# Optimization experiments

Hardware: AMD Instinct MI355X
Metric: run time of the kernel (lower is better)

The kernel has to match this reference:

```python
import jax, jax.numpy as jnp
import numpy as np

ALPHA = 0.2  # LeakyReLU negative slope
B, N, F_IN, F_OUT = 8, 2048, 256, 64


def setup_inputs() -> dict:
    key = jax.random.key(0)
    k1, k2, k3, k4 = jax.random.split(key, 4)
    x = jax.random.normal(k1, (B, N, F_IN), dtype=jnp.float32)
    adj = jax.random.randint(k2, (B, N, N), 0, 2, dtype=jnp.int32)
    # xavier_uniform with gain=1.414
    gain = 1.414
    lim_W = gain * np.sqrt(6.0 / (F_IN + F_OUT))
    W = jax.random.uniform(k3, (F_IN, F_OUT), dtype=jnp.float32, minval=-lim_W, maxval=lim_W)
    lim_a = gain * np.sqrt(6.0 / (2 * F_OUT + 1))
    a = jax.random.uniform(k4, (2 * F_OUT, 1), dtype=jnp.float32, minval=-lim_a, maxval=lim_a)
    return {"x": x, "adj": adj, "W": W, "a": a}


def reference(x, adj, W, a):
    h = jnp.einsum('bni,io->bno', x, W)  # [B, N, F_OUT]
    f_out = W.shape[1]
    # additive score a^T [h_i ; h_j] = (h_i . a_left) + (h_j . a_right)
    a_left = a[:f_out, 0]   # [F_OUT]
    a_right = a[f_out:, 0]  # [F_OUT]
    e_l = h @ a_left   # [B, N]
    e_r = h @ a_right  # [B, N]
    e = e_l[:, :, None] + e_r[:, None, :]          # [B, N, N]
    e = jnp.where(e > 0, e, ALPHA * e)             # LeakyReLU
    e = jnp.where(adj > 0, e, jnp.float32(-9e15))  # adjacency mask
    attention = jax.nn.softmax(e, axis=2)          # [B, N, N]
    h_prime = jnp.einsum('bnm,bmo->bno', attention, h)  # [B, N, F_OUT]
    return jax.nn.elu(h_prime)
```

## Files before the change

kernel.cpp:

```cpp
#include <hip/hip_runtime.h>
#include <math.h>

#define BATCH 8
#define NN 2048
#define FIN 256
#define FOUT 64
#define ALPHA 0.2f

typedef __attribute__((ext_vector_type(8))) short bf16x8;
typedef __attribute__((ext_vector_type(4))) float f32x4;

static __device__ __forceinline__ unsigned short f2bf(float f) {
  unsigned int u = __float_as_uint(f);
  u += 0x7fffu + ((u >> 16) & 1u);
  return (unsigned short)(u >> 16);
}
static __device__ __forceinline__ float bf2f(unsigned short h) {
  return __uint_as_float(((unsigned int)h) << 16);
}
static __device__ __forceinline__ void gload16(const void* g, void* l) {
  __builtin_amdgcn_global_load_lds(
      (const __attribute__((address_space(1))) unsigned int*)g,
      (__attribute__((address_space(3))) unsigned int*)l, 16, 0, 0);
}

__global__ __launch_bounds__(256) void k1_h(
    const float* __restrict__ x, const float* __restrict__ W,
    const float* __restrict__ a, float* __restrict__ el,
    float* __restrict__ er, unsigned char* __restrict__ hS) {
  __shared__ __align__(16) unsigned short lds[32768];
  const int t = threadIdx.x;
  const int wv = t >> 6;
  const int l = t & 63;
  const int l15 = l & 15;
  const int kg = l >> 4;

  {
    const float4* W4 = (const float4*)W;
    #pragma unroll
    for (int i = 0; i < 16; ++i) {
      int f = t + i * 256;
      float4 v = W4[f];
      int k = f >> 4;
      int ob = (f & 15) * 4;
      float vv[4] = {v.x, v.y, v.z, v.w};
      #pragma unroll
      for (int c = 0; c < 4; ++c) {
        int o = ob + c;
        unsigned short hi = f2bf(vv[c]);
        unsigned short lo = f2bf(vv[c] - bf2f(hi));
        int idx = o * 256 + (((k >> 3) ^ (o & 7)) * 8) + (k & 7);
        lds[idx] = hi;
        lds[16384 + idx] = lo;
      }
    }
  }
  __syncthreads();

  const int row = blockIdx.x * 64 + wv * 16 + l15;
  f32x4 acc[4] = {{0.f,0.f,0.f,0.f},{0.f,0.f,0.f,0.f},
                  {0.f,0.f,0.f,0.f},{0.f,0.f,0.f,0.f}};
  const float* xrow = x + (size_t)row * FIN;

  #pragma unroll
  for (int ks = 0; ks < 8; ++ks) {
    int k0 = ks * 32;
    float4 xa = *(const float4*)(xrow + k0 + kg * 8);
    float4 xb = *(const float4*)(xrow + k0 + kg * 8 + 4);
    float xv[8] = {xa.x, xa.y, xa.z, xa.w, xb.x, xb.y, xb.z, xb.w};
    bf16x8 ahi, alo;
    #pragma unroll
    for (int j = 0; j < 8; ++j) {
      unsigned short hi = f2bf(xv[j]);
      unsigned short lo = f2bf(xv[j] - bf2f(hi));
      ahi[j] = (short)hi;
      alo[j] = (short)lo;
    }
    int kgidx = ks * 4 + kg;
    #pragma unroll
    for (int ot = 0; ot < 4; ++ot) {
      int o = ot * 16 + l15;
      int base = o * 256 + ((kgidx ^ (o & 7)) * 8);
      bf16x8 bhi = *(const bf16x8*)&lds[base];
      bf16x8 blo = *(const bf16x8*)&lds[16384 + base];
      acc[ot] = __builtin_amdgcn_mfma_f32_16x16x32_bf16(ahi, bhi, acc[ot], 0, 0, 0);
      acc[ot] = __builtin_amdgcn_mfma_f32_16x16x32_bf16(ahi, blo, acc[ot], 0, 0, 0);
      acc[ot] = __builtin_amdgcn_mfma_f32_16x16x32_bf16(alo, bhi, acc[ot], 0, 0, 0);
    }
  }

  float aLv[4], aRv[4];
  #pragma unroll
  for (int ot = 0; ot < 4; ++ot) {
    aLv[ot] = a[ot * 16 + l15];
    aRv[ot] = a[64 + ot * 16 + l15];
  }
  #pragma unroll
  for (int jj = 0; jj < 4; ++jj) {
    float pl = 0.f, pr = 0.f;
    #pragma unroll
    for (int ot = 0; ot < 4; ++ot) {
      pl += acc[ot][jj] * aLv[ot];
      pr += acc[ot][jj] * aRv[ot];
    }
    #pragma unroll
    for (int s = 1; s < 16; s <<= 1) {
      pl += __shfl_xor(pl, s);
      pr += __shfl_xor(pr, s);
    }
    if (l15 == 0) {
      int grow = blockIdx.x * 64 + wv * 16 + kg * 4 + jj;
      el[grow] = pl;
      er[grow] = pr;
    }
  }

  __syncthreads();
  #pragma unroll
  for (int ot = 0; ot < 4; ++ot) {
    int o = ot * 16 + l15;
    int xorv = (o >> 1) & 3;
    #pragma unroll
    for (int jj = 0; jj < 4; ++jj) {
      int m_loc = wv * 16 + kg * 4 + jj;
      int ks2 = m_loc >> 5;
      int kg2 = (m_loc >> 3) & 3;
      int j = m_loc & 7;
      int kgp = kg2 ^ xorv;
      float v = acc[ot][jj];
      unsigned short hi = f2bf(v);
      unsigned short lo = f2bf(v - bf2f(hi));
      int base = ((ks2 * 2 + 0) * 64 + o) * 32 + kgp * 8 + j;
      lds[base] = hi;
      lds[base + 2048] = lo;
    }
  }
  __syncthreads();

  {
    const uint4* src = (const uint4*)(const void*)lds;
    uint4* dst = (uint4*)(hS + (size_t)blockIdx.x * 16384);
    #pragma unroll
    for (int i = 0; i < 4; ++i) dst[t + i * 256] = src[t + i * 256];
  }
}

__global__ __launch_bounds__(256, 2) void k2_attn(
    const int* __restrict__ adj, const unsigned char* __restrict__ hS,
    const float* __restrict__ el, const float* __restrict__ er,
    float* __restrict__ out) {
  __shared__ __align__(1024) unsigned char buf[2][2][16384];
  const int t = threadIdx.x;
  const int wv = t >> 6;
  const int l = t & 63;
  const int l15 = l & 15;
  const int kg = l >> 4;
  const int pair = wv >> 1;
  const int pw = wv & 1;

  int bid = blockIdx.x;
  int swz = (bid & 7) * 64 + (bid >> 3);
  int b = swz >> 6;
  int n0 = (swz & 63) * 32;
  const int nrow = n0 + pw * 16 + l15;

  const float eL = el[b * NN + nrow];
  const float* erp = er + b * NN + pair * 1024;
  const int* arow = adj + (size_t)b * NN * NN + (size_t)nrow * NN + pair * 1024;
  const unsigned char* hSb =
      hS + (size_t)b * 32 * 16384 + (size_t)pair * 16 * 16384;

  const int laneoff = l15 * 64 + ((kg ^ ((l >> 1) & 3)) * 16);

  f32x4 acc[4] = {{0.f,0.f,0.f,0.f},{0.f,0.f,0.f,0.f},
                  {0.f,0.f,0.f,0.f},{0.f,0.f,0.f,0.f}};
  float Sacc = 0.f;

  #pragma unroll
  for (int s = 0; s < 8; ++s) {
    int seg = pw * 8 + s;
    gload16(hSb + seg * 1024 + l * 16, &buf[pair][0][seg * 1024]);
  }
  int4 av[4];
  float4 ev[4];
  #pragma unroll
  for (int ksx = 0; ksx < 2; ++ksx) {
    av[ksx * 2 + 0] = *(const int4*)(arow + ksx * 32 + kg * 8);
    av[ksx * 2 + 1] = *(const int4*)(arow + ksx * 32 + kg * 8 + 4);
    ev[ksx * 2 + 0] = *(const float4*)(erp + ksx * 32 + kg * 8);
    ev[ksx * 2 + 1] = *(const float4*)(erp + ksx * 32 + kg * 8 + 4);
  }
  __syncthreads();

  for (int tc = 0; tc < 16; ++tc) {
    const unsigned char* cur = &buf[pair][tc & 1][0];
    int4 avn[4];
    float4 evn[4];
    if (tc < 15) {
      const unsigned char* src = hSb + (size_t)(tc + 1) * 16384;
      unsigned char* dstb = &buf[pair][(tc + 1) & 1][0];
      #pragma unroll
      for (int s = 0; s < 8; ++s) {
        int seg = pw * 8 + s;
        gload16(src + seg * 1024 + l * 16, dstb + seg * 1024);
      }
      int mb = (tc + 1) * 64;
      #pragma unroll
      for (int ksx = 0; ksx < 2; ++ksx) {
        avn[ksx * 2 + 0] = *(const int4*)(arow + mb + ksx * 32 + kg * 8);
        avn[ksx * 2 + 1] = *(const int4*)(arow + mb + ksx * 32 + kg * 8 + 4);
        evn[ksx * 2 + 0] = *(const float4*)(erp + mb + ksx * 32 + kg * 8);
        evn[ksx * 2 + 1] = *(const float4*)(erp + mb + ksx * 32 + kg * 8 + 4);
      }
    }

    #pragma unroll
    for (int ks = 0; ks < 2; ++ks) {
      int aarr[8] = {av[ks*2].x, av[ks*2].y, av[ks*2].z, av[ks*2].w,
                     av[ks*2+1].x, av[ks*2+1].y, av[ks*2+1].z, av[ks*2+1].w};
      float earr[8] = {ev[ks*2].x, ev[ks*2].y, ev[ks*2].z, ev[ks*2].w,
                       ev[ks*2+1].x, ev[ks*2+1].y, ev[ks*2+1].z, ev[ks*2+1].w};
      bf16x8 af;
      #pragma unroll
      for (int j = 0; j < 8; ++j) {
        float e = eL + earr[j];
        e = fmaxf(e, ALPHA * e);
        float w = (aarr[j] > 0) ? __expf(e) : 0.f;
        unsigned short hb = f2bf(w);
        af[j] = (short)hb;
        Sacc += bf2f(hb);
      }
      #pragma unroll
      for (int ot = 0; ot < 4; ++ot) {
        const unsigned char* p = cur + ks * 8192 + ot * 1024 + laneoff;
        bf16x8 bhi = *(const bf16x8*)p;
        bf16x8 blo = *(const bf16x8*)(p + 4096);
        acc[ot] = __builtin_amdgcn_mfma_f32_16x16x32_bf16(af, bhi, acc[ot], 0, 0, 0);
        acc[ot] = __builtin_amdgcn_mfma_f32_16x16x32_bf16(af, blo, acc[ot], 0, 0, 0);
      }
    }

    if (tc < 15) {
      #pragma unroll
      for (int i = 0; i < 4; ++i) { av[i] = avn[i]; ev[i] = evn[i]; }
    }
    __syncthreads();
  }

  float Sred = Sacc + __shfl_xor(Sacc, 16);
  Sred += __shfl_xor(Sred, 32);

  {
    unsigned char* cb = &buf[0][0][0];
    const int slot = pw * 64 + l;
    if (pair == 1) {
      float* dst = (float*)(cb + slot * 96);
      *(f32x4*)(dst + 0)  = acc[0];
      *(f32x4*)(dst + 4)  = acc[1];
      *(f32x4*)(dst + 8)  = acc[2];
      *(f32x4*)(dst + 12) = acc[3];
      dst[16] = Sred;
    }
    __syncthreads();
    if (pair == 1) return;
    const float* src = (const float*)(cb + slot * 96);
    #pragma unroll
    for (int ot = 0; ot < 4; ++ot) {
      f32x4 o4 = *(const f32x4*)(src + ot * 4);
      acc[ot] += o4;
    }
    Sred += src[16];
  }

  float Sj[4];
  #pragma unroll
  for (int jj = 0; jj < 4; ++jj) Sj[jj] = __shfl(Sred, kg * 4 + jj);
  #pragma unroll
  for (int ot = 0; ot < 4; ++ot) {
    #pragma unroll
    for (int jj = 0; jj < 4; ++jj) {
      float v = acc[ot][jj] / Sj[jj];
      float res = v > 0.f ? v : expm1f(v);
      out[((size_t)b * NN + n0 + pw * 16 + kg * 4 + jj) * FOUT + ot * 16 + l15] = res;
    }
  }
}

extern "C" void kernel_launch(void* const* d_in, const int* in_sizes, int n_in,
                              void* d_out, int out_size, void* d_ws, size_t ws_size,
                              hipStream_t stream) {
  const float* x   = (const float*)d_in[0];
  const int*   adj = (const int*)d_in[1];
  const float* W   = (const float*)d_in[2];
  const float* a   = (const float*)d_in[3];
  float* out = (float*)d_out;

  unsigned char* hS = (unsigned char*)d_ws;
  float* el = (float*)(hS + (size_t)BATCH * 32 * 16384);
  float* er = el + BATCH * NN;

  hipLaunchKernelGGL(k1_h, dim3(256), dim3(256), 0, stream, x, W, a, el, er, hS);
  hipLaunchKernelGGL(k2_attn, dim3(512), dim3(256), 0, stream, adj, hS, el, er, out);
}
```

Measured before the change: 52.57 us.

## Deepen adjacency/score register prefetch to two stages with manual vmcnt waits

```diff
diff --git a/kernel.cpp b/kernel.cpp
--- a/kernel.cpp
+++ b/kernel.cpp
@@ -176,50 +176,51 @@
                   {0.f,0.f,0.f,0.f},{0.f,0.f,0.f,0.f}};
   float Sacc = 0.f;
 
-  #pragma unroll
-  for (int s = 0; s < 8; ++s) {
-    int seg = pw * 8 + s;
-    gload16(hSb + seg * 1024 + l * 16, &buf[pair][0][seg * 1024]);
-  }
-  int4 av[4];
-  float4 ev[4];
-  #pragma unroll
-  for (int ksx = 0; ksx < 2; ++ksx) {
-    av[ksx * 2 + 0] = *(const int4*)(arow + ksx * 32 + kg * 8);
-    av[ksx * 2 + 1] = *(const int4*)(arow + ksx * 32 + kg * 8 + 4);
-    ev[ksx * 2 + 0] = *(const float4*)(erp + ksx * 32 + kg * 8);
-    ev[ksx * 2 + 1] = *(const float4*)(erp + ksx * 32 + kg * 8 + 4);
-  }
-  __syncthreads();
-
+  int4 av0[4], av1[4], av2[4];
+  float4 ev0[4], ev1[4], ev2[4];
+
+#define STAGE(tcc) {                                                       \
+    const unsigned char* src_ = hSb + (size_t)(tcc) * 16384;               \
+    unsigned char* dst_ = &buf[pair][(tcc) & 1][0];                        \
+    _Pragma("unroll")                                                      \
+    for (int s_ = 0; s_ < 8; ++s_) {                                       \
+      int seg_ = pw * 8 + s_;                                              \
+      gload16(src_ + seg_ * 1024 + l * 16, dst_ + seg_ * 1024);            \
+    } }
+
+#define LOADR(A, E, tcc) {                                                 \
+    int mb_ = (tcc) * 64;                                                  \
+    _Pragma("unroll")                                                      \
+    for (int kx_ = 0; kx_ < 2; ++kx_) {                                    \
+      A[kx_*2+0] = *(const int4*)(arow + mb_ + kx_*32 + kg*8);             \
+      A[kx_*2+1] = *(const int4*)(arow + mb_ + kx_*32 + kg*8 + 4);         \
+      E[kx_*2+0] = *(const float4*)(erp + mb_ + kx_*32 + kg*8);            \
+      E[kx_*2+1] = *(const float4*)(erp + mb_ + kx_*32 + kg*8 + 4);        \
+    } }
+
+  STAGE(0);
+  LOADR(av0, ev0, 0);
+  LOADR(av1, ev1, 1);
+  asm volatile("s_waitcnt vmcnt(0)" ::: "memory");
+  __builtin_amdgcn_s_barrier();
+
+  #pragma unroll
   for (int tc = 0; tc < 16; ++tc) {
+    if (tc < 15) STAGE(tc + 1);
+    if (tc < 14) LOADR(av2, ev2, tc + 2);
+
+    if (tc < 14)      { asm volatile("s_waitcnt vmcnt(16)" ::: "memory"); }
+    else if (tc < 15) { asm volatile("s_waitcnt vmcnt(8)"  ::: "memory"); }
+    else              { asm volatile("s_waitcnt vmcnt(0)"  ::: "memory"); }
+    __builtin_amdgcn_s_barrier();
+
     const unsigned char* cur = &buf[pair][tc & 1][0];
-    int4 avn[4];
-    float4 evn[4];
-    if (tc < 15) {
-      const unsigned char* src = hSb + (size_t)(tc + 1) * 16384;
-      unsigned char* dstb = &buf[pair][(tc + 1) & 1][0];
-      #pragma unroll
-      for (int s = 0; s < 8; ++s) {
-        int seg = pw * 8 + s;
-        gload16(src + seg * 1024 + l * 16, dstb + seg * 1024);
-      }
-      int mb = (tc + 1) * 64;
-      #pragma unroll
-      for (int ksx = 0; ksx < 2; ++ksx) {
-        avn[ksx * 2 + 0] = *(const int4*)(arow + mb + ksx * 32 + kg * 8);
-        avn[ksx * 2 + 1] = *(const int4*)(arow + mb + ksx * 32 + kg * 8 + 4);
-        evn[ksx * 2 + 0] = *(const float4*)(erp + mb + ksx * 32 + kg * 8);
-        evn[ksx * 2 + 1] = *(const float4*)(erp + mb + ksx * 32 + kg * 8 + 4);
-      }
-    }
-
     #pragma unroll
     for (int ks = 0; ks < 2; ++ks) {
-      int aarr[8] = {av[ks*2].x, av[ks*2].y, av[ks*2].z, av[ks*2].w,
-                     av[ks*2+1].x, av[ks*2+1].y, av[ks*2+1].z, av[ks*2+1].w};
-      float earr[8] = {ev[ks*2].x, ev[ks*2].y, ev[ks*2].z, ev[ks*2].w,
-                       ev[ks*2+1].x, ev[ks*2+1].y, ev[ks*2+1].z, ev[ks*2+1].w};
+      int aarr[8] = {av0[ks*2].x, av0[ks*2].y, av0[ks*2].z, av0[ks*2].w,
+                     av0[ks*2+1].x, av0[ks*2+1].y, av0[ks*2+1].z, av0[ks*2+1].w};
+      float earr[8] = {ev0[ks*2].x, ev0[ks*2].y, ev0[ks*2].z, ev0[ks*2].w,
+                       ev0[ks*2+1].x, ev0[ks*2+1].y, ev0[ks*2+1].z, ev0[ks*2+1].w};
       bf16x8 af;
       #pragma unroll
       for (int j = 0; j < 8; ++j) {
@@ -240,11 +241,14 @@
       }
     }
 
-    if (tc < 15) {
-      #pragma unroll
-      for (int i = 0; i < 4; ++i) { av[i] = avn[i]; ev[i] = evn[i]; }
-    }
-    __syncthreads();
+    asm volatile("" ::: "memory");
+    __builtin_amdgcn_s_barrier();
+
+    #pragma unroll
+    for (int i = 0; i < 4; ++i) {
+      av0[i] = av1[i]; ev0[i] = ev1[i];
+      av1[i] = av2[i]; ev1[i] = ev2[i];
+    }
   }
 
   float Sred = Sacc + __shfl_xor(Sacc, 16);
```

New measurement: 56.17 us. 1.07x slower.
